# Kernel optimization log

Hardware: AMD Instinct MI355X
Metric: run time of the kernel (lower is better)

## Reference

```python
import jax, jax.numpy as jnp
import numpy as np

VOCAB = 65
N_EMBD = 32
BLOCK = 8
N_HEADS = 4
HEAD = N_EMBD // N_HEADS  # 8
SQRT_C = float(N_EMBD) ** 0.5  # faithful bug: scores are MULTIPLIED by sqrt(n_embd)


def setup_inputs() -> dict:
    key = jax.random.key(0)
    ks = jax.random.split(key, 12)
    B, T = 65536, 8
    idx = jax.random.randint(ks[0], (B, T), 0, VOCAB, dtype=jnp.int64 if jax.config.jax_enable_x64 else jnp.int32)
    targets = jax.random.randint(ks[1], (B, T), 0, VOCAB, dtype=idx.dtype)
    s = 1.0 / np.sqrt(N_EMBD)
    return {
        "idx": idx,
        "targets": targets,
        "tok_emb": jax.random.normal(ks[2], (VOCAB, N_EMBD), jnp.float32),
        "pos_emb": jax.random.normal(ks[3], (BLOCK, N_EMBD), jnp.float32),
        # per-head Q/K/V projections stacked: [n_heads, n_embd, head_size]
        "Wq": jax.random.normal(ks[4], (N_HEADS, N_EMBD, HEAD), jnp.float32) * s,
        "Wk": jax.random.normal(ks[5], (N_HEADS, N_EMBD, HEAD), jnp.float32) * s,
        "Wv": jax.random.normal(ks[6], (N_HEADS, N_EMBD, HEAD), jnp.float32) * s,
        "W_mlp": jax.random.normal(ks[7], (N_EMBD, N_EMBD), jnp.float32) * s,
        "b_mlp": jnp.zeros((N_EMBD,), jnp.float32),
        "W_lm": jax.random.normal(ks[8], (N_EMBD, VOCAB), jnp.float32) * s,
        "b_lm": jnp.zeros((VOCAB,), jnp.float32),
    }


def reference(idx, targets, tok_emb, pos_emb, Wq, Wk, Wv, W_mlp, b_mlp, W_lm, b_lm):
    B, T = idx.shape
    x = tok_emb[idx] + pos_emb[:T]                       # [B,T,C]
    q = jnp.einsum('btc,hcd->bhtd', x, Wq)               # [B,H,T,D]
    k = jnp.einsum('btc,hcd->bhtd', x, Wk)
    v = jnp.einsum('btc,hcd->bhtd', x, Wv)
    wei = jnp.einsum('bhtd,bhsd->bhts', q, k) * SQRT_C   # faithful: * C**0.5
    tril = jnp.tril(jnp.ones((T, T), bool))
    wei = jnp.where(tril, wei, -jnp.inf)
    wei = jax.nn.softmax(wei, axis=-1)
    out = jnp.einsum('bhts,bhsd->bhtd', wei, v)          # [B,H,T,D]
    x = out.transpose(0, 2, 1, 3).reshape(B, T, N_EMBD)  # concat heads
    x = jax.nn.relu(x @ W_mlp + b_mlp)                   # MLP
    logits = x @ W_lm + b_lm                             # [B,T,V]
    logits = logits.reshape(B * T, VOCAB)
    logp = jax.nn.log_softmax(logits, axis=-1)
    tgt = targets.reshape(B * T)
    loss = -jnp.take_along_axis(logp, tgt[:, None], axis=-1).mean()
    return logits, loss
```

## Files before the change

### kernel.cpp

```cpp
#include <hip/hip_runtime.h>
#include <hip/hip_bf16.h>

#define VOCAB   65
#define SQRT_C  5.656854249492381f
#define BATCHES 65536
#define ROWS    (BATCHES * 8)
#define TABSZ   (8 * VOCAB * 32)
#define PAIRS   (BATCHES / 2)
#define NBLOCKS 2048
#define NWAVES  (NBLOCKS * 4)
#define NFRAG   448

typedef __attribute__((ext_vector_type(8))) short  short8;
typedef __attribute__((ext_vector_type(4))) float  float4v;

__device__ __forceinline__ void wave_fence() {
    __asm__ volatile("s_waitcnt lgkmcnt(0)" ::: "memory");
}
__device__ __forceinline__ short bfbits(float f) {
    __hip_bfloat16 h = __float2bfloat16(f);
    return *reinterpret_cast<short*>(&h);
}

__global__ void qkv_table_kernel(const float* __restrict__ tok_emb,
                                 const float* __restrict__ pos_emb,
                                 const float* __restrict__ Wq,
                                 const float* __restrict__ Wk,
                                 const float* __restrict__ Wv,
                                 const float* __restrict__ W_mlp,
                                 const float* __restrict__ W_lm,
                                 float* __restrict__ qtab,
                                 float* __restrict__ ktab,
                                 float* __restrict__ vtab,
                                 float* __restrict__ frag_tab,
                                 float* __restrict__ loss_acc) {
    int o = blockIdx.x * 256 + threadIdx.x;
    if (o == 0) loss_acc[0] = 0.f;

    if (o < 3 * TABSZ) {
        int table = o / TABSZ;
        int r = o - table * TABSZ;
        int pair = r >> 5;
        int cd = r & 31;
        int t = pair / VOCAB;
        int tok = pair - t * VOCAB;
        int h = cd >> 3, d = cd & 7;
        const float* W = (table == 0) ? Wq : (table == 1) ? Wk : Wv;
        float acc = 0.f;
        #pragma unroll
        for (int c = 0; c < 32; ++c) {
            float xc = tok_emb[tok * 32 + c] + pos_emb[t * 32 + c];
            acc += xc * W[h * 256 + c * 8 + d];
        }
        if (table == 0) acc *= SQRT_C;
        float* tab = (table == 0) ? qtab : (table == 1) ? ktab : vtab;
        tab[r] = acc;
    } else if (o < 3 * TABSZ + NFRAG) {
        int f = o - 3 * TABSZ;
        int cls = f >> 6, lane = f & 63;
        int q4l = lane >> 4, nl = lane & 15;
        short8 v;
        #pragma unroll
        for (int j = 0; j < 8; ++j) {
            int k = q4l * 8 + j;
            if (cls < 2)       v[j] = bfbits(W_mlp[k * 32 + cls * 16 + nl]);
            else if (cls < 6)  v[j] = bfbits(W_lm[k * VOCAB + (cls - 2) * 16 + nl]);
            else               v[j] = (nl == 0) ? bfbits(W_lm[k * VOCAB + 64]) : (short)0;
        }
        ((short8*)frag_tab)[f] = v;
    }
}

__global__ __launch_bounds__(256) void fused_kernel(
        const int* __restrict__ idx, const int* __restrict__ targets,
        const float* __restrict__ qtab, const float* __restrict__ ktab,
        const float* __restrict__ vtab,
        const float* __restrict__ frag_tab,
        const float* __restrict__ b_mlp,
        const float* __restrict__ b_lm,
        float* __restrict__ out_logits,
        float* __restrict__ loss_acc) {
    __shared__ __align__(16) float sK[4][544];
    __shared__ __align__(16) float sV[4][544];
    __shared__ __align__(16) unsigned short sX3[4][640];

    const int tid = threadIdx.x;
    const int w = tid >> 6, l = tid & 63;
    const int q4 = l >> 4;
    const int n  = l & 15;
    const int t  = l & 7, b2 = (l >> 3) & 1, h = q4;

    const short8* ftab = (const short8*)frag_tab;
    short8 wmf[2], wlf[4], wlf4;
    wmf[0] = ftab[l];        wmf[1] = ftab[64 + l];
    #pragma unroll
    for (int c = 0; c < 4; ++c) wlf[c] = ftab[(2 + c) * 64 + l];
    wlf4 = ftab[6 * 64 + l];
    float bmc[2], blc[4];
    #pragma unroll
    for (int c = 0; c < 2; ++c) bmc[c] = b_mlp[c * 16 + n];
    #pragma unroll
    for (int c = 0; c < 4; ++c) blc[c] = b_lm[c * 16 + n];
    const float bl64 = b_lm[64];
    const float4v zf = {0.f, 0.f, 0.f, 0.f};

    float loss_local = 0.f;

    int pb = blockIdx.x * 4 + w;
    int tokv = 0, tgv = 0;
    if (l < 16) { tokv = idx[pb * 16 + l]; tgv = targets[pb * 16 + l]; }

    for (; pb < PAIRS; pb += NWAVES) {
        #pragma unroll
        for (int half = 0; half < 2; ++half) {
            int c = l + half * 64;
            int d2 = c & 1, s = (c >> 1) & 7, grp = c >> 4;
            int b2g = grp & 1, hg = grp >> 1;
            int tok_s = __shfl(tokv, b2g * 8 + s);
            int gaddr = (s * VOCAB + tok_s) * 32 + hg * 8 + d2 * 4;
            int laddr = grp * 68 + s * 8 + d2 * 4;
            *(float4*)(&sK[w][laddr]) = *(const float4*)(ktab + gaddr);
            *(float4*)(&sV[w][laddr]) = *(const float4*)(vtab + gaddr);
        }
        int tok_t = __shfl(tokv, b2 * 8 + t);
        const float* qp = qtab + (t * VOCAB + tok_t) * 32 + h * 8;
        const float4 q0 = *(const float4*)(qp);
        const float4 q1 = *(const float4*)(qp + 4);
        int tgrc[4];
        #pragma unroll
        for (int i = 0; i < 4; ++i) tgrc[i] = __shfl(tgv, q4 * 4 + i);

        const int pbn = pb + NWAVES;
        int tokv_n = 0, tgv_n = 0;
        if (pbn < PAIRS && l < 16) {
            tokv_n = idx[pbn * 16 + l];
            tgv_n  = targets[pbn * 16 + l];
        }
        wave_fence();

        const float* kb = &sK[w][(h * 2 + b2) * 68];
        const float* vb = &sV[w][(h * 2 + b2) * 68];
        float sc[8], m = -1e30f;
        #pragma unroll
        for (int s = 0; s < 8; ++s) {
            float4 k0 = *(const float4*)(kb + s * 8);
            float4 k1 = *(const float4*)(kb + s * 8 + 4);
            float d = q0.x * k0.x + q0.y * k0.y + q0.z * k0.z + q0.w * k0.w
                    + q1.x * k1.x + q1.y * k1.y + q1.z * k1.z + q1.w * k1.w;
            sc[s] = d;
            if (s <= t) m = fmaxf(m, d);
        }
        float p[8], sum = 0.f;
        #pragma unroll
        for (int s = 0; s < 8; ++s) {
            p[s] = (s <= t) ? __expf(sc[s] - m) : 0.f;
            sum += p[s];
        }
        float inv = 1.f / sum;
        float o[8];
        #pragma unroll
        for (int d = 0; d < 8; ++d) o[d] = 0.f;
        #pragma unroll
        for (int s = 0; s < 8; ++s) {
            float4 v0 = *(const float4*)(vb + s * 8);
            float4 v1 = *(const float4*)(vb + s * 8 + 4);
            o[0] += p[s] * v0.x; o[1] += p[s] * v0.y;
            o[2] += p[s] * v0.z; o[3] += p[s] * v0.w;
            o[4] += p[s] * v1.x; o[5] += p[s] * v1.y;
            o[6] += p[s] * v1.z; o[7] += p[s] * v1.w;
        }
        short8 a2;
        #pragma unroll
        for (int d = 0; d < 8; ++d) a2[d] = bfbits(o[d] * inv);

        float4v d0 = __builtin_amdgcn_mfma_f32_16x16x32_bf16(a2, wmf[0], zf, 0, 0, 0);
        float4v d1 = __builtin_amdgcn_mfma_f32_16x16x32_bf16(a2, wmf[1], zf, 0, 0, 0);
        #pragma unroll
        for (int i = 0; i < 4; ++i) {
            int row = q4 * 4 + i;
            sX3[w][row * 40 + n]      = (unsigned short)bfbits(fmaxf(d0[i] + bmc[0], 0.f));
            sX3[w][row * 40 + 16 + n] = (unsigned short)bfbits(fmaxf(d1[i] + bmc[1], 0.f));
        }
        wave_fence();
        short8 a3 = *(const short8*)(&sX3[w][n * 40 + q4 * 8]);

        float4v Lc[4];
        #pragma unroll
        for (int c = 0; c < 4; ++c)
            Lc[c] = __builtin_amdgcn_mfma_f32_16x16x32_bf16(a3, wlf[c], zf, 0, 0, 0);
        float4v L64 = __builtin_amdgcn_mfma_f32_16x16x32_bf16(a3, wlf4, zf, 0, 0, 0);

        size_t rb = (size_t)pb * 16;
        float part[4] = {0.f, 0.f, 0.f, 0.f};
        #pragma unroll
        for (int c = 0; c < 4; ++c) {
            #pragma unroll
            for (int i = 0; i < 4; ++i) {
                float Lv = Lc[c][i] + blc[c];
                out_logits[(rb + q4 * 4 + i) * VOCAB + c * 16 + n] = Lv;
                part[i] += __expf(Lv);
                if (c * 16 + n == tgrc[i]) loss_local -= Lv;
            }
        }
        if (n == 0) {
            #pragma unroll
            for (int i = 0; i < 4; ++i) {
                float Lv = L64[i] + bl64;
                out_logits[(rb + q4 * 4 + i) * VOCAB + 64] = Lv;
                part[i] += __expf(Lv);
                if (tgrc[i] == 64) loss_local -= Lv;
            }
        }
        #pragma unroll
        for (int off = 1; off < 16; off <<= 1) {
            #pragma unroll
            for (int i = 0; i < 4; ++i) part[i] += __shfl_xor(part[i], off);
        }
        if (n == 0)
            loss_local += __logf(part[0]) + __logf(part[1])
                        + __logf(part[2]) + __logf(part[3]);

        tokv = tokv_n; tgv = tgv_n;
    }

    #pragma unroll
    for (int off = 1; off < 64; off <<= 1) loss_local += __shfl_xor(loss_local, off);
    if (l == 0) atomicAdd(loss_acc, loss_local);
}

__global__ void finalize_loss(const float* __restrict__ acc,
                              float* __restrict__ out) {
    out[0] = acc[0] * (1.f / (float)ROWS);
}

extern "C" void kernel_launch(void* const* d_in, const int* in_sizes, int n_in,
                              void* d_out, int out_size, void* d_ws, size_t ws_size,
                              hipStream_t stream) {
    const int* idx        = (const int*)d_in[0];
    const int* targets    = (const int*)d_in[1];
    const float* tok_emb  = (const float*)d_in[2];
    const float* pos_emb  = (const float*)d_in[3];
    const float* Wq       = (const float*)d_in[4];
    const float* Wk       = (const float*)d_in[5];
    const float* Wv       = (const float*)d_in[6];
    const float* W_mlp    = (const float*)d_in[7];
    const float* b_mlp    = (const float*)d_in[8];
    const float* W_lm     = (const float*)d_in[9];
    const float* b_lm     = (const float*)d_in[10];
    float* out            = (float*)d_out;

    float* ws        = (float*)d_ws;
    float* loss_ptr  = ws;
    float* frag      = ws + 16;
    float* qtab      = frag + 1792;
    float* ktab      = qtab + TABSZ;
    float* vtab      = ktab + TABSZ;
    float* out_loss  = out + (size_t)ROWS * VOCAB;

    qkv_table_kernel<<<(3 * TABSZ + NFRAG + 255) / 256, 256, 0, stream>>>(
        tok_emb, pos_emb, Wq, Wk, Wv, W_mlp, W_lm,
        qtab, ktab, vtab, frag, loss_ptr);

    fused_kernel<<<NBLOCKS, 256, 0, stream>>>(
        idx, targets, qtab, ktab, vtab, frag, b_mlp, b_lm, out, loss_ptr);

    finalize_loss<<<1, 1, 0, stream>>>(loss_ptr, out_loss);
}
```

Baseline: 363.8 us.

## Launch one wave per batch pair instead of a persistent grid-stride loop

The persistent grid-stride loop with software prefetch of the next pair's tokens is removed. The kernel now launches PAIRS/4 blocks, each wave handling exactly one pair, with launch bounds set to target 8 blocks per CU. The sX3 scratch buffer is aliased onto sK to cut LDS use. Loss reduction now goes through per-block shared sums and 16 spread atomic slots instead of one atomic per wave on a single address, trading less atomic contention for more block launches and weight-fragment reloads per pair.

```diff
diff --git a/kernel.cpp b/kernel.cpp
--- a/kernel.cpp
+++ b/kernel.cpp
@@ -7,8 +7,7 @@
 #define ROWS    (BATCHES * 8)
 #define TABSZ   (8 * VOCAB * 32)
 #define PAIRS   (BATCHES / 2)
-#define NBLOCKS 2048
-#define NWAVES  (NBLOCKS * 4)
+#define NBLOCKS (PAIRS / 4)
 #define NFRAG   448
 
 typedef __attribute__((ext_vector_type(8))) short  short8;
@@ -33,9 +32,9 @@
                                  float* __restrict__ ktab,
                                  float* __restrict__ vtab,
                                  float* __restrict__ frag_tab,
-                                 float* __restrict__ loss_acc) {
+                                 float* __restrict__ loss_slots) {
     int o = blockIdx.x * 256 + threadIdx.x;
-    if (o == 0) loss_acc[0] = 0.f;
+    if (o < 16) loss_slots[o * 16] = 0.f;
 
     if (o < 3 * TABSZ) {
         int table = o / TABSZ;
@@ -71,7 +70,7 @@
     }
 }
 
-__global__ __launch_bounds__(256) void fused_kernel(
+__global__ __launch_bounds__(256, 8) void fused_kernel(
         const int* __restrict__ idx, const int* __restrict__ targets,
         const float* __restrict__ qtab, const float* __restrict__ ktab,
         const float* __restrict__ vtab,
@@ -79,10 +78,10 @@
         const float* __restrict__ b_mlp,
         const float* __restrict__ b_lm,
         float* __restrict__ out_logits,
-        float* __restrict__ loss_acc) {
+        float* __restrict__ loss_slots) {
     __shared__ __align__(16) float sK[4][544];
     __shared__ __align__(16) float sV[4][544];
-    __shared__ __align__(16) unsigned short sX3[4][640];
+    __shared__ float wsum[4];
 
     const int tid = threadIdx.x;
     const int w = tid >> 6, l = tid & 63;
@@ -90,6 +89,11 @@
     const int n  = l & 15;
     const int t  = l & 7, b2 = (l >> 3) & 1, h = q4;
 
+    const int pb = blockIdx.x * 4 + w;
+
+    int tokv = 0, tgv = 0;
+    if (l < 16) { tokv = idx[pb * 16 + l]; tgv = targets[pb * 16 + l]; }
+
     const short8* ftab = (const short8*)frag_tab;
     short8 wmf[2], wlf[4], wlf4;
     wmf[0] = ftab[l];        wmf[1] = ftab[64 + l];
@@ -104,133 +108,125 @@
     const float bl64 = b_lm[64];
     const float4v zf = {0.f, 0.f, 0.f, 0.f};
 
+    #pragma unroll
+    for (int half = 0; half < 2; ++half) {
+        int c = l + half * 64;
+        int d2 = c & 1, s = (c >> 1) & 7, grp = c >> 4;
+        int b2g = grp & 1, hg = grp >> 1;
+        int tok_s = __shfl(tokv, b2g * 8 + s);
+        int gaddr = (s * VOCAB + tok_s) * 32 + hg * 8 + d2 * 4;
+        int laddr = grp * 68 + s * 8 + d2 * 4;
+        *(float4*)(&sK[w][laddr]) = *(const float4*)(ktab + gaddr);
+        *(float4*)(&sV[w][laddr]) = *(const float4*)(vtab + gaddr);
+    }
+    const int tok_t = __shfl(tokv, b2 * 8 + t);
+    const float* qp = qtab + (t * VOCAB + tok_t) * 32 + h * 8;
+    const float4 q0 = *(const float4*)(qp);
+    const float4 q1 = *(const float4*)(qp + 4);
+    int tgrc[4];
+    #pragma unroll
+    for (int i = 0; i < 4; ++i) tgrc[i] = __shfl(tgv, q4 * 4 + i);
+    wave_fence();
+
+    const float* kb = &sK[w][(h * 2 + b2) * 68];
+    const float* vb = &sV[w][(h * 2 + b2) * 68];
+    float sc[8], m = -1e30f;
+    #pragma unroll
+    for (int s = 0; s < 8; ++s) {
+        float4 k0 = *(const float4*)(kb + s * 8);
+        float4 k1 = *(const float4*)(kb + s * 8 + 4);
+        float d = q0.x * k0.x + q0.y * k0.y + q0.z * k0.z + q0.w * k0.w
+                + q1.x * k1.x + q1.y * k1.y + q1.z * k1.z + q1.w * k1.w;
+        sc[s] = d;
+        if (s <= t) m = fmaxf(m, d);
+    }
+    float p[8], sum = 0.f;
+    #pragma unroll
+    for (int s = 0; s < 8; ++s) {
+        p[s] = (s <= t) ? __expf(sc[s] - m) : 0.f;
+        sum += p[s];
+    }
+    float inv = 1.f / sum;
+    float o[8];
+    #pragma unroll
+    for (int d = 0; d < 8; ++d) o[d] = 0.f;
+    #pragma unroll
+    for (int s = 0; s < 8; ++s) {
+        float4 v0 = *(const float4*)(vb + s * 8);
+        float4 v1 = *(const float4*)(vb + s * 8 + 4);
+        o[0] += p[s] * v0.x; o[1] += p[s] * v0.y;
+        o[2] += p[s] * v0.z; o[3] += p[s] * v0.w;
+        o[4] += p[s] * v1.x; o[5] += p[s] * v1.y;
+        o[6] += p[s] * v1.z; o[7] += p[s] * v1.w;
+    }
+    short8 a2;
+    #pragma unroll
+    for (int d = 0; d < 8; ++d) a2[d] = bfbits(o[d] * inv);
+
+    float4v d0 = __builtin_amdgcn_mfma_f32_16x16x32_bf16(a2, wmf[0], zf, 0, 0, 0);
+    float4v d1 = __builtin_amdgcn_mfma_f32_16x16x32_bf16(a2, wmf[1], zf, 0, 0, 0);
+    unsigned short* sx3 = (unsigned short*)(&sK[w][0]);
+    #pragma unroll
+    for (int i = 0; i < 4; ++i) {
+        int row = q4 * 4 + i;
+        sx3[row * 40 + n]      = (unsigned short)bfbits(fmaxf(d0[i] + bmc[0], 0.f));
+        sx3[row * 40 + 16 + n] = (unsigned short)bfbits(fmaxf(d1[i] + bmc[1], 0.f));
+    }
+    wave_fence();
+    short8 a3 = *(const short8*)(&sx3[n * 40 + q4 * 8]);
+
+    float4v Lc[4];
+    #pragma unroll
+    for (int c = 0; c < 4; ++c)
+        Lc[c] = __builtin_amdgcn_mfma_f32_16x16x32_bf16(a3, wlf[c], zf, 0, 0, 0);
+    float4v L64 = __builtin_amdgcn_mfma_f32_16x16x32_bf16(a3, wlf4, zf, 0, 0, 0);
+
     float loss_local = 0.f;
-
-    int pb = blockIdx.x * 4 + w;
-    int tokv = 0, tgv = 0;
-    if (l < 16) { tokv = idx[pb * 16 + l]; tgv = targets[pb * 16 + l]; }
-
-    for (; pb < PAIRS; pb += NWAVES) {
-        #pragma unroll
-        for (int half = 0; half < 2; ++half) {
-            int c = l + half * 64;
-            int d2 = c & 1, s = (c >> 1) & 7, grp = c >> 4;
-            int b2g = grp & 1, hg = grp >> 1;
-            int tok_s = __shfl(tokv, b2g * 8 + s);
-            int gaddr = (s * VOCAB + tok_s) * 32 + hg * 8 + d2 * 4;
-            int laddr = grp * 68 + s * 8 + d2 * 4;
-            *(float4*)(&sK[w][laddr]) = *(const float4*)(ktab + gaddr);
-            *(float4*)(&sV[w][laddr]) = *(const float4*)(vtab + gaddr);
-        }
-        int tok_t = __shfl(tokv, b2 * 8 + t);
-        const float* qp = qtab + (t * VOCAB + tok_t) * 32 + h * 8;
-        const float4 q0 = *(const float4*)(qp);
-        const float4 q1 = *(const float4*)(qp + 4);
-        int tgrc[4];
-        #pragma unroll
-        for (int i = 0; i < 4; ++i) tgrc[i] = __shfl(tgv, q4 * 4 + i);
-
-        const int pbn = pb + NWAVES;
-        int tokv_n = 0, tgv_n = 0;
-        if (pbn < PAIRS && l < 16) {
-            tokv_n = idx[pbn * 16 + l];
-            tgv_n  = targets[pbn * 16 + l];
-        }
-        wave_fence();
-
-        const float* kb = &sK[w][(h * 2 + b2) * 68];
-        const float* vb = &sV[w][(h * 2 + b2) * 68];
-        float sc[8], m = -1e30f;
-        #pragma unroll
-        for (int s = 0; s < 8; ++s) {
-            float4 k0 = *(const float4*)(kb + s * 8);
-            float4 k1 = *(const float4*)(kb + s * 8 + 4);
-            float d = q0.x * k0.x + q0.y * k0.y + q0.z * k0.z + q0.w * k0.w
-                    + q1.x * k1.x + q1.y * k1.y + q1.z * k1.z + q1.w * k1.w;
-            sc[s] = d;
-            if (s <= t) m = fmaxf(m, d);
-        }
-        float p[8], sum = 0.f;
-        #pragma unroll
-        for (int s = 0; s < 8; ++s) {
-            p[s] = (s <= t) ? __expf(sc[s] - m) : 0.f;
-            sum += p[s];
-        }
-        float inv = 1.f / sum;
-        float o[8];
-        #pragma unroll
-        for (int d = 0; d < 8; ++d) o[d] = 0.f;
-        #pragma unroll
-        for (int s = 0; s < 8; ++s) {
-            float4 v0 = *(const float4*)(vb + s * 8);
-            float4 v1 = *(const float4*)(vb + s * 8 + 4);
-            o[0] += p[s] * v0.x; o[1] += p[s] * v0.y;
-            o[2] += p[s] * v0.z; o[3] += p[s] * v0.w;
-            o[4] += p[s] * v1.x; o[5] += p[s] * v1.y;
-            o[6] += p[s] * v1.z; o[7] += p[s] * v1.w;
-        }
-        short8 a2;
-        #pragma unroll
-        for (int d = 0; d < 8; ++d) a2[d] = bfbits(o[d] * inv);
-
-        float4v d0 = __builtin_amdgcn_mfma_f32_16x16x32_bf16(a2, wmf[0], zf, 0, 0, 0);
-        float4v d1 = __builtin_amdgcn_mfma_f32_16x16x32_bf16(a2, wmf[1], zf, 0, 0, 0);
+    size_t rb = (size_t)pb * 16;
+    float part[4] = {0.f, 0.f, 0.f, 0.f};
+    #pragma unroll
+    for (int c = 0; c < 4; ++c) {
         #pragma unroll
         for (int i = 0; i < 4; ++i) {
-            int row = q4 * 4 + i;
-            sX3[w][row * 40 + n]      = (unsigned short)bfbits(fmaxf(d0[i] + bmc[0], 0.f));
-            sX3[w][row * 40 + 16 + n] = (unsigned short)bfbits(fmaxf(d1[i] + bmc[1], 0.f));
-        }
-        wave_fence();
-        short8 a3 = *(const short8*)(&sX3[w][n * 40 + q4 * 8]);
-
-        float4v Lc[4];
-        #pragma unroll
-        for (int c = 0; c < 4; ++c)
-            Lc[c] = __builtin_amdgcn_mfma_f32_16x16x32_bf16(a3, wlf[c], zf, 0, 0, 0);
-        float4v L64 = __builtin_amdgcn_mfma_f32_16x16x32_bf16(a3, wlf4, zf, 0, 0, 0);
-
-        size_t rb = (size_t)pb * 16;
-        float part[4] = {0.f, 0.f, 0.f, 0.f};
-        #pragma unroll
-        for (int c = 0; c < 4; ++c) {
-            #pragma unroll
-            for (int i = 0; i < 4; ++i) {
-                float Lv = Lc[c][i] + blc[c];
-                out_logits[(rb + q4 * 4 + i) * VOCAB + c * 16 + n] = Lv;
-                part[i] += __expf(Lv);
-                if (c * 16 + n == tgrc[i]) loss_local -= Lv;
-            }
-        }
-        if (n == 0) {
-            #pragma unroll
-            for (int i = 0; i < 4; ++i) {
-                float Lv = L64[i] + bl64;
-                out_logits[(rb + q4 * 4 + i) * VOCAB + 64] = Lv;
-                part[i] += __expf(Lv);
-                if (tgrc[i] == 64) loss_local -= Lv;
-            }
-        }
-        #pragma unroll
-        for (int off = 1; off < 16; off <<= 1) {
-            #pragma unroll
-            for (int i = 0; i < 4; ++i) part[i] += __shfl_xor(part[i], off);
-        }
-        if (n == 0)
-            loss_local += __logf(part[0]) + __logf(part[1])
-                        + __logf(part[2]) + __logf(part[3]);
-
-        tokv = tokv_n; tgv = tgv_n;
-    }
+            float Lv = Lc[c][i] + blc[c];
+            out_logits[(rb + q4 * 4 + i) * VOCAB + c * 16 + n] = Lv;
+            part[i] += __expf(Lv);
+            if (c * 16 + n == tgrc[i]) loss_local -= Lv;
+        }
+    }
+    if (n == 0) {
+        #pragma unroll
+        for (int i = 0; i < 4; ++i) {
+            float Lv = L64[i] + bl64;
+            out_logits[(rb + q4 * 4 + i) * VOCAB + 64] = Lv;
+            part[i] += __expf(Lv);
+            if (tgrc[i] == 64) loss_local -= Lv;
+        }
+    }
+    #pragma unroll
+    for (int off = 1; off < 16; off <<= 1) {
+        #pragma unroll
+        for (int i = 0; i < 4; ++i) part[i] += __shfl_xor(part[i], off);
+    }
+    if (n == 0)
+        loss_local += __logf(part[0]) + __logf(part[1])
+                    + __logf(part[2]) + __logf(part[3]);
 
     #pragma unroll
     for (int off = 1; off < 64; off <<= 1) loss_local += __shfl_xor(loss_local, off);
-    if (l == 0) atomicAdd(loss_acc, loss_local);
-}
-
-__global__ void finalize_loss(const float* __restrict__ acc,
+    if (l == 0) wsum[w] = loss_local;
+    __syncthreads();
+    if (tid == 0)
+        atomicAdd(&loss_slots[(blockIdx.x & 15) * 16],
+                  wsum[0] + wsum[1] + wsum[2] + wsum[3]);
+}
+
+__global__ void finalize_loss(const float* __restrict__ slots,
                               float* __restrict__ out) {
-    out[0] = acc[0] * (1.f / (float)ROWS);
+    float tot = 0.f;
+    #pragma unroll
+    for (int s = 0; s < 16; ++s) tot += slots[s * 16];
+    out[0] = tot * (1.f / (float)ROWS);
 }
 
 extern "C" void kernel_launch(void* const* d_in, const int* in_sizes, int n_in,
@@ -249,20 +245,20 @@
     const float* b_lm     = (const float*)d_in[10];
     float* out            = (float*)d_out;
 
-    float* ws        = (float*)d_ws;
-    float* loss_ptr  = ws;
-    float* frag      = ws + 16;
-    float* qtab      = frag + 1792;
-    float* ktab      = qtab + TABSZ;
-    float* vtab      = ktab + TABSZ;
-    float* out_loss  = out + (size_t)ROWS * VOCAB;
+    float* ws         = (float*)d_ws;
+    float* loss_slots = ws;
+    float* frag       = ws + 256;
+    float* qtab       = frag + 1792;
+    float* ktab       = qtab + TABSZ;
+    float* vtab       = ktab + TABSZ;
+    float* out_loss   = out + (size_t)ROWS * VOCAB;
 
     qkv_table_kernel<<<(3 * TABSZ + NFRAG + 255) / 256, 256, 0, stream>>>(
         tok_emb, pos_emb, Wq, Wk, Wv, W_mlp, W_lm,
-        qtab, ktab, vtab, frag, loss_ptr);
+        qtab, ktab, vtab, frag, loss_slots);
 
     fused_kernel<<<NBLOCKS, 256, 0, stream>>>(
-        idx, targets, qtab, ktab, vtab, frag, b_mlp, b_lm, out, loss_ptr);
-
-    finalize_loss<<<1, 1, 0, stream>>>(loss_ptr, out_loss);
-}
+        idx, targets, qtab, ktab, vtab, frag, b_mlp, b_lm, out, loss_slots);
+
+    finalize_loss<<<1, 1, 0, stream>>>(loss_slots, out_loss);
+}
```

Result: faster. 336.5 us (-7.5%).
